# Kernel optimization log

Hardware: AMD Instinct MI355X
Metric: run time of the kernel (lower is better)

The kernel has to match this reference:

```python
import jax, jax.numpy as jnp
import numpy as np

EMBED_DIM = 512
NUM_HEADS = 8
Q1, Q2 = 0, 96    # hardcoded query slice in source (104-8)
K1, K2 = 96, 104  # hardcoded key/value slice in source


def prelu(x, a):
    # nn.PReLU() with a single shared parameter (init 0.25)
    return jnp.where(x >= 0, x, a * x)


def setup_inputs() -> dict:
    key = jax.random.key(0)
    k1, k2, k3, k4 = jax.random.split(key, 4)
    E = EMBED_DIM
    ipt = jax.random.normal(k1, (104, 1024, E), dtype=jnp.float32)
    # torch Linear weights are [out_features, in_features]; y = x @ W.T
    s = 1.0 / np.sqrt(E)
    Wq = jax.random.uniform(k2, (E, E), jnp.float32, -s, s)
    Wkv = jax.random.uniform(k3, (2 * E, E), jnp.float32, -s, s)
    Wpost = jax.random.uniform(k4, (E, E), jnp.float32, -s, s)
    prelu_a = jnp.float32(0.25)
    return {"ipt": ipt, "Wq": Wq, "Wkv": Wkv, "Wpost": Wpost, "prelu_a": prelu_a}


def reference(ipt, Wq, Wkv, Wpost, prelu_a):
    S, B, E = ipt.shape
    H = NUM_HEADS
    dh = E // H
    Sq = Q2 - Q1
    Sk = K2 - K1

    q = prelu(ipt[Q1:Q2] @ Wq.T, prelu_a)              # [Sq, B, E]
    kv = prelu(ipt[K1:K2] @ Wkv.T, prelu_a)            # [Sk, B, 2E]
    k, v = kv[..., :E], kv[..., E:]                     # [Sk, B, E] each

    # [S, B, E] -> [S, B*H, dh] -> [B*H, S, dh]
    q = q.reshape(Sq, B * H, dh).transpose(1, 0, 2)
    k = k.reshape(Sk, B * H, dh).transpose(1, 0, 2)
    v = v.reshape(Sk, B * H, dh).transpose(1, 0, 2)

    attn = jnp.einsum('bqd,bkd->bqk', q, k)            # [B*H, Sq, Sk]
    # data-dependent zero mask: scores exactly equal to 0 get -10000
    attn = (attn + jnp.where(attn == 0, jnp.float32(-10000.0), jnp.float32(0.0)))
    # NB: scale uses FULL embed_dim (source reassigns emb_dim from q.shape)
    attn = attn * (E ** -0.5)

    # global softmax over flattened Sq*Sk per (batch*head)
    attn_sm = jax.nn.softmax(attn.reshape(B * H, Sq * Sk), axis=-1)
    attn_sm = attn_sm.reshape(B * H, Sq, Sk)

    out = jnp.einsum('bqk,bkd->bqd', attn_sm, v)       # [B*H, Sq, dh]
    out = out.transpose(1, 0, 2).reshape(Sq, B, E)     # [Sq, B, E]
    out = out @ Wpost.T

    attn_sm_mean = attn_sm.reshape(B, H, Sq, Sk).mean(axis=1)
    attn_mean = attn.reshape(B, H, Sq, Sk).mean(axis=1)
    return out, attn_sm_mean, attn_mean
```

## Files before the change

kernel.cpp:

```cpp
#include <hip/hip_runtime.h>
#include <hip/hip_bf16.h>

typedef unsigned int u32;
typedef unsigned short u16;
typedef __attribute__((ext_vector_type(8))) short bf16x8;
typedef __attribute__((ext_vector_type(4))) float f32x4;

#define MEAN_SM  50331648ll
#define MEAN_AT  51118080ll
#define KV_OFF    0ll
#define WQ_OFF    8388608ll
#define WKV_OFF   8650752ll
#define WPOST_OFF 9175040ll

__device__ __forceinline__ u16 f2bf(float x){
  u32 u = __float_as_uint(x);
  return (u16)((u + 0x7fffu + ((u >> 16) & 1u)) >> 16);
}
__device__ __forceinline__ float bf2f(u32 s){ return __uint_as_float(s << 16); }
__device__ __forceinline__ u32 cvt2(float x, float y){
  __hip_bfloat162 h = __float22bfloat162_rn(make_float2(x, y));
  u32 r; __builtin_memcpy(&r, &h, 4); return r;
}

__global__ __launch_bounds__(256)
void conv_bf16(const float* __restrict__ src, u16* __restrict__ dst, int n8)
{
  int c = blockIdx.x * 256 + threadIdx.x;
  if (c < n8) {
    float4 f0 = *reinterpret_cast<const float4*>(src + (size_t)c * 8);
    float4 f1 = *reinterpret_cast<const float4*>(src + (size_t)c * 8 + 4);
    uint4 p = make_uint4(cvt2(f0.x, f0.y), cvt2(f0.z, f0.w),
                         cvt2(f1.x, f1.y), cvt2(f1.z, f1.w));
    *reinterpret_cast<uint4*>(dst + (size_t)c * 8) = p;
  }
}

template<int OBF16, int PRELU>
__global__ __launch_bounds__(256)
void mfma_gemm(const float* __restrict__ A, const u16* __restrict__ Wb,
               void* __restrict__ Cout, int N, const float* __restrict__ paPtr)
{
  __shared__ u16 lA[128][72];
  __shared__ u16 lW[128][72];
  const int tid  = threadIdx.x;
  const int lane = tid & 63;
  const int wr   = (tid >> 7) & 1;
  const int wc   = (tid >> 6) & 1;
  const int lr   = lane & 15;
  const int lk   = (lane >> 4) << 3;
  const size_t m0 = (size_t)blockIdx.y * 128;
  const int n0 = blockIdx.x * 128;

  const f32x4 zero = {0.f, 0.f, 0.f, 0.f};
  f32x4 acc[4][4];
#pragma unroll
  for (int i = 0; i < 4; ++i)
#pragma unroll
    for (int j = 0; j < 4; ++j) acc[i][j] = zero;

  for (int k0 = 0; k0 < 512; k0 += 64) {
#pragma unroll
    for (int i = 0; i < 8; ++i) {
      int c = tid + i * 256;
      int row = c >> 4;
      int k4  = (c & 15) << 2;
      float4 f = *reinterpret_cast<const float4*>(A + (m0 + row) * 512 + k0 + k4);
      *reinterpret_cast<uint2*>(&lA[row][k4]) =
          make_uint2(cvt2(f.x, f.y), cvt2(f.z, f.w));
    }
#pragma unroll
    for (int i = 0; i < 4; ++i) {
      int c = tid + i * 256;
      int row = c >> 3;
      int k8  = (c & 7) << 3;
      *reinterpret_cast<uint4*>(&lW[row][k8]) =
          *reinterpret_cast<const uint4*>(Wb + (size_t)(n0 + row) * 512 + k0 + k8);
    }
    __syncthreads();
#pragma unroll
    for (int ks = 0; ks < 2; ++ks) {
      bf16x8 af[4], bw[4];
#pragma unroll
      for (int t = 0; t < 4; ++t) {
        af[t] = *reinterpret_cast<const bf16x8*>(&lA[wr * 64 + t * 16 + lr][ks * 32 + lk]);
        bw[t] = *reinterpret_cast<const bf16x8*>(&lW[wc * 64 + t * 16 + lr][ks * 32 + lk]);
      }
#pragma unroll
      for (int mi = 0; mi < 4; ++mi)
#pragma unroll
        for (int nj = 0; nj < 4; ++nj)
          acc[mi][nj] = __builtin_amdgcn_mfma_f32_16x16x32_bf16(af[mi], bw[nj], acc[mi][nj], 0, 0, 0);
    }
    __syncthreads();
  }

  const float pa = PRELU ? paPtr[0] : 0.0f;
#pragma unroll
  for (int mi = 0; mi < 4; ++mi)
#pragma unroll
    for (int nj = 0; nj < 4; ++nj) {
#pragma unroll
      for (int j = 0; j < 4; ++j) {
        size_t r = m0 + wr * 64 + mi * 16 + ((lane >> 4) << 2) + j;
        int cc = n0 + wc * 64 + nj * 16 + lr;
        float x = acc[mi][nj][j];
        if (PRELU && x < 0.f) x *= pa;
        if (OBF16) ((u16*)Cout)[r * (size_t)N + cc] = f2bf(x);
        else       ((float*)Cout)[r * (size_t)N + cc] = x;
      }
    }
}

__global__ __launch_bounds__(256)
void attn_kernel(const u16* __restrict__ KVb, float* __restrict__ O)
{
  const int b   = blockIdx.x;
  const int tid = threadIdx.x;

  __shared__ float kv[8][1028];
  __shared__ float qh[96][68];
  __shared__ float sc[96][8];
  __shared__ float am[768];
  __shared__ float asmv[768];
  __shared__ float red[4];

#pragma unroll
  for (int i = 0; i < 4; ++i) {
    int c = tid + i * 256;
    int sk = c >> 7;
    int j8 = (c & 127) << 3;
    uint4 u = *reinterpret_cast<const uint4*>(KVb + ((size_t)(sk * 1024 + b)) * 1024 + j8);
    kv[sk][j8 + 0] = bf2f(u.x & 0xffffu); kv[sk][j8 + 1] = bf2f(u.x >> 16);
    kv[sk][j8 + 2] = bf2f(u.y & 0xffffu); kv[sk][j8 + 3] = bf2f(u.y >> 16);
    kv[sk][j8 + 4] = bf2f(u.z & 0xffffu); kv[sk][j8 + 5] = bf2f(u.z >> 16);
    kv[sk][j8 + 6] = bf2f(u.w & 0xffffu); kv[sk][j8 + 7] = bf2f(u.w >> 16);
  }
  for (int idx = tid; idx < 768; idx += 256) { am[idx] = 0.0f; asmv[idx] = 0.0f; }
  __syncthreads();

  const float scale = 0.04419417382415922f;

  for (int h = 0; h < 8; ++h) {
#pragma unroll
    for (int r = 0; r < 6; ++r) {
      int idx = tid + r * 256;
      int q  = idx >> 4;
      int d4 = (idx & 15) << 2;
      float4 u = *reinterpret_cast<const float4*>(O + ((size_t)(q * 1024 + b)) * 512 + h * 64 + d4);
      qh[q][d4 + 0] = u.x; qh[q][d4 + 1] = u.y;
      qh[q][d4 + 2] = u.z; qh[q][d4 + 3] = u.w;
    }
    __syncthreads();

    float s[3];
#pragma unroll
    for (int r = 0; r < 3; ++r) {
      int idx = tid + r * 256;
      int q  = idx >> 3;
      int kk = idx & 7;
      float a = 0.0f;
#pragma unroll
      for (int d = 0; d < 64; d += 4) {
        float4 qa = *reinterpret_cast<const float4*>(&qh[q][d]);
        float4 ka = *reinterpret_cast<const float4*>(&kv[kk][h * 64 + d]);
        a += qa.x * ka.x + qa.y * ka.y + qa.z * ka.z + qa.w * ka.w;
      }
      if (a == 0.0f) a -= 10000.0f;
      s[r] = a * scale;
      am[idx] += s[r] * 0.125f;
    }

    float mx = fmaxf(fmaxf(s[0], s[1]), s[2]);
#pragma unroll
    for (int off = 32; off; off >>= 1) mx = fmaxf(mx, __shfl_xor(mx, off));
    if ((tid & 63) == 0) red[tid >> 6] = mx;
    __syncthreads();
    const float Mx = fmaxf(fmaxf(red[0], red[1]), fmaxf(red[2], red[3]));
    __syncthreads();

    float e0 = __expf(s[0] - Mx), e1 = __expf(s[1] - Mx), e2 = __expf(s[2] - Mx);
    float ls = e0 + e1 + e2;
#pragma unroll
    for (int off = 32; off; off >>= 1) ls += __shfl_xor(ls, off);
    if ((tid & 63) == 0) red[tid >> 6] = ls;
    __syncthreads();
    const float T = red[0] + red[1] + red[2] + red[3];
    const float inv = 1.0f / T;

    {
      float sm0 = e0 * inv, sm1 = e1 * inv, sm2 = e2 * inv;
      int i0 = tid, i1 = tid + 256, i2 = tid + 512;
      sc[i0 >> 3][i0 & 7] = sm0;
      sc[i1 >> 3][i1 & 7] = sm1;
      sc[i2 >> 3][i2 & 7] = sm2;
      asmv[i0] += sm0 * 0.125f;
      asmv[i1] += sm1 * 0.125f;
      asmv[i2] += sm2 * 0.125f;
    }
    __syncthreads();

#pragma unroll
    for (int r = 0; r < 12; ++r) {
      int idx = tid + r * 256;
      int q  = idx >> 5;
      int d2 = (idx & 31) << 1;
      float a0 = 0.0f, a1 = 0.0f;
#pragma unroll
      for (int kk = 0; kk < 8; ++kk) {
        float smv = sc[q][kk];
        a0 += smv * kv[kk][512 + h * 64 + d2];
        a1 += smv * kv[kk][512 + h * 64 + d2 + 1];
      }
      float2 pk; pk.x = a0; pk.y = a1;
      *reinterpret_cast<float2*>(O + ((size_t)(q * 1024 + b)) * 512 + h * 64 + d2) = pk;
    }
    __syncthreads();
  }

  const size_t base1 = MEAN_SM + (size_t)b * 768;
  const size_t base2 = MEAN_AT + (size_t)b * 768;
  for (int idx = tid; idx < 768; idx += 256) {
    O[base1 + idx] = asmv[idx];
    O[base2 + idx] = am[idx];
  }
}

__global__ __launch_bounds__(512)
void post_gemm(float* __restrict__ C, const u16* __restrict__ Wb)
{
  __shared__ u16 lA[64][40];
  __shared__ u16 lW[512][40];
  const int tid  = threadIdx.x;
  const int lane = tid & 63;
  const int w    = tid >> 6;
  const int lr   = lane & 15;
  const int lk   = (lane >> 4) << 3;
  const size_t m0 = (size_t)blockIdx.x * 64;

  const f32x4 zero = {0.f, 0.f, 0.f, 0.f};
  f32x4 acc[4][4];
#pragma unroll
  for (int i = 0; i < 4; ++i)
#pragma unroll
    for (int j = 0; j < 4; ++j) acc[i][j] = zero;

  for (int k0 = 0; k0 < 512; k0 += 32) {
    {
      int row = tid >> 3;
      int k4  = (tid & 7) << 2;
      float4 f = *reinterpret_cast<const float4*>(C + (m0 + row) * 512 + k0 + k4);
      *reinterpret_cast<uint2*>(&lA[row][k4]) =
          make_uint2(cvt2(f.x, f.y), cvt2(f.z, f.w));
    }
#pragma unroll
    for (int i = 0; i < 4; ++i) {
      int c = tid + i * 512;
      int n  = c >> 2;
      int k8 = (c & 3) << 3;
      *reinterpret_cast<uint4*>(&lW[n][k8]) =
          *reinterpret_cast<const uint4*>(Wb + (size_t)n * 512 + k0 + k8);
    }
    __syncthreads();
    bf16x8 af[4], bw[4];
#pragma unroll
    for (int t = 0; t < 4; ++t) {
      af[t] = *reinterpret_cast<const bf16x8*>(&lA[t * 16 + lr][lk]);
      bw[t] = *reinterpret_cast<const bf16x8*>(&lW[w * 64 + t * 16 + lr][lk]);
    }
#pragma unroll
    for (int mi = 0; mi < 4; ++mi)
#pragma unroll
      for (int nj = 0; nj < 4; ++nj)
        acc[mi][nj] = __builtin_amdgcn_mfma_f32_16x16x32_bf16(af[mi], bw[nj], acc[mi][nj], 0, 0, 0);
    __syncthreads();
  }

#pragma unroll
  for (int mi = 0; mi < 4; ++mi)
#pragma unroll
    for (int nj = 0; nj < 4; ++nj) {
#pragma unroll
      for (int j = 0; j < 4; ++j) {
        size_t r = m0 + mi * 16 + ((lane >> 4) << 2) + j;
        int cc = w * 64 + nj * 16 + lr;
        C[r * 512 + cc] = acc[mi][nj][j];
      }
    }
}

extern "C" void kernel_launch(void* const* d_in, const int* in_sizes, int n_in,
                              void* d_out, int out_size, void* d_ws, size_t ws_size,
                              hipStream_t stream)
{
  (void)in_sizes; (void)n_in; (void)out_size; (void)ws_size;
  const float* ipt   = (const float*)d_in[0];
  const float* Wq    = (const float*)d_in[1];
  const float* Wkv   = (const float*)d_in[2];
  const float* Wpost = (const float*)d_in[3];
  const float* pa    = (const float*)d_in[4];
  float* out = (float*)d_out;
  u16*   wsb = (u16*)d_ws;

  conv_bf16<<<128, 256, 0, stream>>>(Wq,    wsb + WQ_OFF,    32768);
  conv_bf16<<<256, 256, 0, stream>>>(Wkv,   wsb + WKV_OFF,   65536);
  conv_bf16<<<128, 256, 0, stream>>>(Wpost, wsb + WPOST_OFF, 32768);

  mfma_gemm<0, 1><<<dim3(4, 768), 256, 0, stream>>>(ipt, wsb + WQ_OFF, out, 512, pa);
  mfma_gemm<1, 1><<<dim3(8, 64), 256, 0, stream>>>(ipt + 50331648ll, wsb + WKV_OFF,
                                                   wsb + KV_OFF, 1024, pa);
  attn_kernel<<<1024, 256, 0, stream>>>(wsb + KV_OFF, out);
  post_gemm<<<1536, 512, 0, stream>>>(out, wsb + WPOST_OFF);
}
```

Baseline: 640.4 us.

## Store Q and attention intermediates as bf16 in output rows; swizzle Q GEMM blocks

The Q projection and the attention output are now written as bf16 into the first half of each 2048-byte output row, replacing fp32 values. This halves the intermediate traffic between the Q GEMM, the attention kernel and the post GEMM, and lets post_gemm load its A operand without converting it. The Q GEMM also gets a 1D grid with a block swizzle so that neighbouring blocks share A rows, which should improve L2 reuse. The cost is one more bf16 rounding on attention scores and outputs, although post_gemm already rounded its input to bf16, and the in-place reuse of output rows needs careful ordering.

New measurement: 621.7 us. -2.9%, faster.

```diff
diff --git a/kernel.cpp b/kernel.cpp
--- a/kernel.cpp
+++ b/kernel.cpp
@@ -12,6 +12,7 @@
 #define WQ_OFF    8388608ll
 #define WKV_OFF   8650752ll
 #define WPOST_OFF 9175040ll
+#define SLOT 2048ll
 
 __device__ __forceinline__ u16 f2bf(float x){
   u32 u = __float_as_uint(x);
@@ -36,21 +37,30 @@
   }
 }
 
-template<int OBF16, int PRELU>
+template<int OMODE, int PRELU, int SWZ>
 __global__ __launch_bounds__(256)
 void mfma_gemm(const float* __restrict__ A, const u16* __restrict__ Wb,
                void* __restrict__ Cout, int N, const float* __restrict__ paPtr)
 {
   __shared__ u16 lA[128][72];
   __shared__ u16 lW[128][72];
+  int bx, by;
+  if (SWZ) {
+    int L = blockIdx.x;
+    int x = L & 7;
+    int j = L >> 3;
+    by = x * 96 + (j >> 2);
+    bx = j & 3;
+  } else { bx = blockIdx.x; by = blockIdx.y; }
+
   const int tid  = threadIdx.x;
   const int lane = tid & 63;
   const int wr   = (tid >> 7) & 1;
   const int wc   = (tid >> 6) & 1;
   const int lr   = lane & 15;
   const int lk   = (lane >> 4) << 3;
-  const size_t m0 = (size_t)blockIdx.y * 128;
-  const int n0 = blockIdx.x * 128;
+  const size_t m0 = (size_t)by * 128;
+  const int n0 = bx * 128;
 
   const f32x4 zero = {0.f, 0.f, 0.f, 0.f};
   f32x4 acc[4][4];
@@ -106,14 +116,14 @@
         int cc = n0 + wc * 64 + nj * 16 + lr;
         float x = acc[mi][nj][j];
         if (PRELU && x < 0.f) x *= pa;
-        if (OBF16) ((u16*)Cout)[r * (size_t)N + cc] = f2bf(x);
-        else       ((float*)Cout)[r * (size_t)N + cc] = x;
+        if (OMODE == 1) ((u16*)Cout)[r * (size_t)N + cc] = f2bf(x);
+        else            ((u16*)((char*)Cout + r * SLOT))[cc] = f2bf(x);
       }
     }
 }
 
 __global__ __launch_bounds__(256)
-void attn_kernel(const u16* __restrict__ KVb, float* __restrict__ O)
+void attn_kernel(const u16* __restrict__ KVb, char* __restrict__ Ob)
 {
   const int b   = blockIdx.x;
   const int tid = threadIdx.x;
@@ -147,9 +157,10 @@
       int idx = tid + r * 256;
       int q  = idx >> 4;
       int d4 = (idx & 15) << 2;
-      float4 u = *reinterpret_cast<const float4*>(O + ((size_t)(q * 1024 + b)) * 512 + h * 64 + d4);
-      qh[q][d4 + 0] = u.x; qh[q][d4 + 1] = u.y;
-      qh[q][d4 + 2] = u.z; qh[q][d4 + 3] = u.w;
+      const u16* qrow = (const u16*)(Ob + ((size_t)(q * 1024 + b)) * SLOT);
+      uint2 u = *reinterpret_cast<const uint2*>(qrow + h * 64 + d4);
+      qh[q][d4 + 0] = bf2f(u.x & 0xffffu); qh[q][d4 + 1] = bf2f(u.x >> 16);
+      qh[q][d4 + 2] = bf2f(u.y & 0xffffu); qh[q][d4 + 3] = bf2f(u.y >> 16);
     }
     __syncthreads();
 
@@ -212,22 +223,23 @@
         a0 += smv * kv[kk][512 + h * 64 + d2];
         a1 += smv * kv[kk][512 + h * 64 + d2 + 1];
       }
-      float2 pk; pk.x = a0; pk.y = a1;
-      *reinterpret_cast<float2*>(O + ((size_t)(q * 1024 + b)) * 512 + h * 64 + d2) = pk;
-    }
-    __syncthreads();
-  }
-
+      u16* orow = (u16*)(Ob + ((size_t)(q * 1024 + b)) * SLOT);
+      *reinterpret_cast<u32*>(orow + h * 64 + d2) = cvt2(a0, a1);
+    }
+    __syncthreads();
+  }
+
+  float* Of = (float*)Ob;
   const size_t base1 = MEAN_SM + (size_t)b * 768;
   const size_t base2 = MEAN_AT + (size_t)b * 768;
   for (int idx = tid; idx < 768; idx += 256) {
-    O[base1 + idx] = asmv[idx];
-    O[base2 + idx] = am[idx];
+    Of[base1 + idx] = asmv[idx];
+    Of[base2 + idx] = am[idx];
   }
 }
 
 __global__ __launch_bounds__(512)
-void post_gemm(float* __restrict__ C, const u16* __restrict__ Wb)
+void post_gemm(char* __restrict__ Cb, const u16* __restrict__ Wb)
 {
   __shared__ u16 lA[64][40];
   __shared__ u16 lW[512][40];
@@ -249,9 +261,9 @@
     {
       int row = tid >> 3;
       int k4  = (tid & 7) << 2;
-      float4 f = *reinterpret_cast<const float4*>(C + (m0 + row) * 512 + k0 + k4);
+      const u16* arow = (const u16*)(Cb + (m0 + row) * SLOT);
       *reinterpret_cast<uint2*>(&lA[row][k4]) =
-          make_uint2(cvt2(f.x, f.y), cvt2(f.z, f.w));
+          *reinterpret_cast<const uint2*>(arow + k0 + k4);
     }
 #pragma unroll
     for (int i = 0; i < 4; ++i) {
@@ -284,7 +296,7 @@
       for (int j = 0; j < 4; ++j) {
         size_t r = m0 + mi * 16 + ((lane >> 4) << 2) + j;
         int cc = w * 64 + nj * 16 + lr;
-        C[r * 512 + cc] = acc[mi][nj][j];
+        ((float*)(Cb + r * SLOT))[cc] = acc[mi][nj][j];
       }
     }
 }
@@ -299,16 +311,16 @@
   const float* Wkv   = (const float*)d_in[2];
   const float* Wpost = (const float*)d_in[3];
   const float* pa    = (const float*)d_in[4];
-  float* out = (float*)d_out;
-  u16*   wsb = (u16*)d_ws;
+  char*  outB = (char*)d_out;
+  u16*   wsb  = (u16*)d_ws;
 
   conv_bf16<<<128, 256, 0, stream>>>(Wq,    wsb + WQ_OFF,    32768);
   conv_bf16<<<256, 256, 0, stream>>>(Wkv,   wsb + WKV_OFF,   65536);
   conv_bf16<<<128, 256, 0, stream>>>(Wpost, wsb + WPOST_OFF, 32768);
 
-  mfma_gemm<0, 1><<<dim3(4, 768), 256, 0, stream>>>(ipt, wsb + WQ_OFF, out, 512, pa);
-  mfma_gemm<1, 1><<<dim3(8, 64), 256, 0, stream>>>(ipt + 50331648ll, wsb + WKV_OFF,
-                                                   wsb + KV_OFF, 1024, pa);
-  attn_kernel<<<1024, 256, 0, stream>>>(wsb + KV_OFF, out);
-  post_gemm<<<1536, 512, 0, stream>>>(out, wsb + WPOST_OFF);
-}
+  mfma_gemm<2, 1, 1><<<3072, 256, 0, stream>>>(ipt, wsb + WQ_OFF, outB, 512, pa);
+  mfma_gemm<1, 1, 0><<<dim3(8, 64), 256, 0, stream>>>(ipt + 50331648ll, wsb + WKV_OFF,
+                                                      wsb + KV_OFF, 1024, pa);
+  attn_kernel<<<1024, 256, 0, stream>>>(wsb + KV_OFF, outB);
+  post_gemm<<<1536, 512, 0, stream>>>(outB, wsb + WPOST_OFF);
+}
```
